# Kernel optimization log

Measured on AMD Instinct MI355X. Metric: run time of the kernel, lower is better.

The kernel has to match this reference:

```python
import jax, jax.numpy as jnp
import numpy as np

N, K, CI, CO = 1024, 16, 32, 32


def _elu(x):
    return jnp.where(x > 0, x, jnp.expm1(x))


def _eq22(adj, W, b):
    # adj: [B, D, m, m]; W: [15, D, S]; 15 permutation-equivariant basis ops (Maron et al.)
    B, D, m, _ = adj.shape
    mf = jnp.asarray(m, adj.dtype)
    eye = jnp.eye(m, dtype=adj.dtype)
    diag = jnp.diagonal(adj, axis1=2, axis2=3)          # [B,D,m]
    sr = adj.sum(3) / mf                                 # row sums
    sc = adj.sum(2) / mf                                 # col sums
    sd = diag.sum(-1) / mf                               # [B,D]
    sa = adj.sum((2, 3)) / (mf * mf)                     # [B,D]
    full = adj.shape
    bc = lambda t: jnp.broadcast_to(t, full)
    d2m = lambda v: v[..., :, None] * eye
    s2d = lambda s: s[..., None, None] * eye
    s2a = lambda s: jnp.broadcast_to(s[..., None, None], full)
    ops = jnp.stack([
        d2m(diag), s2d(sd), d2m(sr), d2m(sc), s2d(sa),
        bc(sc[..., None, :]), bc(sr[..., None, :]),
        bc(sc[..., :, None]), bc(sr[..., :, None]),
        adj, jnp.swapaxes(adj, 2, 3),
        bc(diag[..., None, :]), bc(diag[..., :, None]),
        s2a(sd), s2a(sa),
    ])  # [15,B,D,m,m]
    return jnp.einsum('pds,pbdij->bsij', W, ops) + b[None, :, None, None]


def _eq21(adj, W, b):
    # adj: [B,D,m,m] -> [B,S,m]; 5 basis ops
    m = adj.shape[-1]
    mf = jnp.asarray(m, adj.dtype)
    diag = jnp.diagonal(adj, axis1=2, axis2=3)
    sr = adj.sum(3) / mf
    sc = adj.sum(2) / mf
    sd = diag.sum(-1) / mf
    sa = adj.sum((2, 3)) / (mf * mf)
    vshape = diag.shape
    ops = jnp.stack([
        diag, sr, sc,
        jnp.broadcast_to(sd[..., None], vshape),
        jnp.broadcast_to(sa[..., None], vshape),
    ])
    return jnp.einsum('pds,pbdi->bsi', W, ops) + b[None, :, None]


def _eq12(x, W, b):
    # x: [B,D,m] -> [B,S,m,m]; 5 basis ops
    B, D, m = x.shape
    mf = jnp.asarray(m, x.dtype)
    eye = jnp.eye(m, dtype=x.dtype)
    s = x.sum(-1) / mf
    full = (B, D, m, m)
    ops = jnp.stack([
        x[..., :, None] * eye,
        s[..., None, None] * eye,
        jnp.broadcast_to(x[..., None, :], full),
        jnp.broadcast_to(x[..., :, None], full),
        jnp.broadcast_to(s[..., None, None], full),
    ])
    return jnp.einsum('pds,pbdij->bsij', W, ops) + b[None, :, None, None]


def _eq11(x, W, b):
    # x: [B,D,m] -> [B,S,m]; 2 basis ops
    mf = jnp.asarray(x.shape[-1], x.dtype)
    s = x.sum(-1) / mf
    ops = jnp.stack([x, jnp.broadcast_to(s[..., None], x.shape)])
    return jnp.einsum('pds,pbdi->bsi', W, ops) + b[None, :, None]


def _forward(x1, A, w22, b22, w21, b21, w12, b12, w11, b11, nbrs):
    n = x1.shape[0]
    # subgraph extraction: gather per-node neighbor features and dense sub-adjacency
    x_sub = jnp.transpose(x1[nbrs], (0, 2, 1))                                      # [N,Ci,K]
    adj_sub = jnp.transpose(A[nbrs[:, :, None], nbrs[:, None, :]], (0, 3, 1, 2))    # [N,Ci,K,K]
    adj_o = jnp.concatenate([_eq22(adj_sub, w22, b22), _eq12(x_sub, w12, b12)], axis=1)  # [N,2S,K,K]
    x_o = jnp.concatenate([_eq21(adj_sub, w21, b21), _eq11(x_sub, w11, b11)], axis=1)    # [N,2S,K]
    c2 = adj_o.shape[1]
    # scatter-mean subgraph edges back to global edge id = src*n + dst
    eid = (nbrs[:, :, None] * n + nbrs[:, None, :]).reshape(-1)
    ev = jnp.transpose(adj_o, (0, 2, 3, 1)).reshape(-1, c2)
    esum = jax.ops.segment_sum(ev, eid, num_segments=n * n)
    ecnt = jax.ops.segment_sum(jnp.ones(eid.shape, ev.dtype), eid, num_segments=n * n)
    edge_attr = _elu(esum / jnp.maximum(ecnt, 1.0)[:, None])
    # scatter-mean subgraph nodes back to global nodes
    nid = nbrs.reshape(-1)
    nv = jnp.transpose(x_o, (0, 2, 1)).reshape(-1, c2)
    nsum = jax.ops.segment_sum(nv, nid, num_segments=n)
    ncnt = jax.ops.segment_sum(jnp.ones(nid.shape, nv.dtype), nid, num_segments=n)
    x_nodes = _elu(nsum / jnp.maximum(ncnt, 1.0)[:, None])
    return edge_attr, x_nodes


def setup_inputs() -> dict:
    key = jax.random.key(0)
    ks = jax.random.split(key, 12)
    return {
        'x1': jax.random.normal(ks[0], (N, CI), jnp.float32),
        'A': jax.random.normal(ks[1], (N, N, CI), jnp.float32),
        'w22': jax.random.normal(ks[2], (15, CI, CO), jnp.float32) * 0.1,
        'b22': jax.random.normal(ks[3], (CO,), jnp.float32) * 0.1,
        'w21': jax.random.normal(ks[4], (5, CI, CO), jnp.float32) * 0.1,
        'b21': jax.random.normal(ks[5], (CO,), jnp.float32) * 0.1,
        'w12': jax.random.normal(ks[6], (5, CI, CO), jnp.float32) * 0.1,
        'b12': jax.random.normal(ks[7], (CO,), jnp.float32) * 0.1,
        'w11': jax.random.normal(ks[8], (2, CI, CO), jnp.float32) * 0.1,
        'b11': jax.random.normal(ks[9], (CO,), jnp.float32) * 0.1,
        'nbrs': jax.random.randint(ks[10], (N, K), 0, N),
    }


def reference(x1, A, w22, b22, w21, b21, w12, b12, w11, b11, nbrs):
    return _forward(x1, A, w22, b22, w21, b21, w12, b12, w11, b11, nbrs)
```

## Files before the change

kernel.cpp:

```cpp
#include <hip/hip_runtime.h>
#include <hip/hip_bf16.h>

#define NN 1024
#define KK 16
#define CI_ 32
#define CO_ 32
#define CAP 64
#define ECAP 8
#define DCAP 128
#define WLCAP 262144

__device__ __forceinline__ float elu_f(float x) {
    return x > 0.0f ? x : expm1f(x);
}

#define ECNT_OFF   0
#define DCNT_OFF   (1024*1024)
#define INVCNT_OFF (DCNT_OFF + 1024)
#define WLCNT_OFF  (INVCNT_OFF + 1024)
#define INVBUF_OFF (WLCNT_OFF + 1024)
#define WL_OFF     (INVBUF_OFF + 1024*CAP)
#define EBUF_OFF   (WL_OFF + WLCAP)
#define DBUF_OFF   (EBUF_OFF + 1024*1024*ECAP)
#define XSTG_OFF   (DBUF_OFF + 1024*DCAP)
#define ASTG_OFF   (XSTG_OFF + 1024*1024)

__global__ __launch_bounds__(256, 2) void subgraph_kernel(
    const float* __restrict__ x1, const float* __restrict__ A,
    const float* __restrict__ w22, const float* __restrict__ b22,
    const float* __restrict__ w21, const float* __restrict__ b21,
    const float* __restrict__ w12, const float* __restrict__ b12,
    const float* __restrict__ w11, const float* __restrict__ b11,
    const int* __restrict__ nbrs,
    float* __restrict__ adj_stage, float* __restrict__ x_stage,
    unsigned int* __restrict__ ecnt, unsigned int* __restrict__ dcnt,
    unsigned int* __restrict__ invcnt, unsigned int* __restrict__ invbuf,
    unsigned int* __restrict__ ebuf, unsigned int* __restrict__ dbuf,
    unsigned int* __restrict__ wlcnt, unsigned int* __restrict__ wl)
{
    const int b = blockIdx.x;
    const int t = threadIdx.x;

    __shared__ float adjS[32][257];
    __shared__ float xS[32][17];
    __shared__ float w10L[32][32];
    __shared__ float w11L[32][32];
    __shared__ float diagL[32][17], srL[32][17], scL[32][17];
    __shared__ float sdL[32], saL[32], sxL[32];
    __shared__ float rowp[32][17], colp[32][17], diagp[32][17];
    __shared__ float constp[32], dconst22[32];
    __shared__ float xi12[32][17], xj12[32][17], d12t[32][17];
    __shared__ float c12[32], dconst12[32];
    __shared__ float o21[32][17], o11[32][17];
    __shared__ int u[16];

    if (t < 16) u[t] = nbrs[b * KK + t];
    __syncthreads();

    if (t < 16) {
        unsigned int pos = atomicAdd(invcnt + u[t], 1u);
        if (pos < CAP) invbuf[(unsigned)u[t] * CAP + pos] = ((unsigned)b << 4) | (unsigned)t;
    }
    {
        const int pi = t >> 4, pj = t & 15;
        const unsigned vv = (unsigned)u[pi], ww = (unsigned)u[pj];
        const unsigned src = (unsigned)b * 256u + (unsigned)t;
        if (vv == ww) {
            unsigned pos = atomicAdd(dcnt + vv, 1u);
            if (pos < DCAP) dbuf[vv * DCAP + pos] = src;
        } else {
            const unsigned eid = vv * NN + ww;
            unsigned pos = atomicAdd(ecnt + eid, 1u);
            if (pos < ECAP) ebuf[(size_t)eid * ECAP + pos] = src;
            if (pos == 0u) {
                unsigned slot = atomicAdd(wlcnt, 1u);
                if (slot < WLCAP) wl[slot] = eid;
            }
        }
    }

    {
        const int pi = t >> 4, pj = t & 15;
        const float4* arow = reinterpret_cast<const float4*>(
            A + ((size_t)u[pi] * NN + (size_t)u[pj]) * CI_);
        #pragma unroll
        for (int q = 0; q < 8; ++q) {
            float4 r = arow[q];
            adjS[4*q+0][t] = r.x; adjS[4*q+1][t] = r.y;
            adjS[4*q+2][t] = r.z; adjS[4*q+3][t] = r.w;
        }
    }
    if (t < 128) {
        const int xi = t >> 3, q = t & 7;
        float4 v = reinterpret_cast<const float4*>(x1 + (size_t)u[xi] * CI_)[q];
        xS[4*q+0][xi] = v.x; xS[4*q+1][xi] = v.y;
        xS[4*q+2][xi] = v.z; xS[4*q+3][xi] = v.w;
    }
    for (int k = t; k < 1024; k += 256) {
        const int d = k >> 5, s = k & 31;
        w10L[d][s] = w22[9  * 1024 + k];
        w11L[d][s] = w22[10 * 1024 + k];
    }
    __syncthreads();

    {
        const int d = t & 31;
        for (int ii = t >> 5; ii < 16; ii += 8) {
            float s_r = 0.f, s_c = 0.f;
            #pragma unroll
            for (int jj = 0; jj < 16; ++jj) {
                s_r += adjS[d][ii * 16 + jj];
                s_c += adjS[d][jj * 16 + ii];
            }
            srL[d][ii] = s_r * (1.f / 16.f);
            scL[d][ii] = s_c * (1.f / 16.f);
            diagL[d][ii] = adjS[d][ii * 16 + ii];
        }
    }
    __syncthreads();
    if (t < 32) {
        float a = 0.f, dd = 0.f, xx = 0.f;
        #pragma unroll
        for (int ii = 0; ii < 16; ++ii) {
            a += srL[t][ii]; dd += diagL[t][ii]; xx += xS[t][ii];
        }
        saL[t] = a * (1.f / 16.f);
        sdL[t] = dd * (1.f / 16.f);
        sxL[t] = xx * (1.f / 16.f);
    }
    __syncthreads();

    {
        const int s = t & 31;
        for (int ii = t >> 5; ii < 16; ii += 8) {
            {
                float rp = 0.f, cp = 0.f, dp = 0.f, o21v = 0.f;
                #pragma unroll 4
                for (int d = 0; d < 32; ++d) {
                    const int wi = d * 32 + s;
                    const float di = diagL[d][ii], sr_ = srL[d][ii], sc_ = scL[d][ii];
                    rp   += w22[7*1024 + wi]*sc_ + w22[8*1024 + wi]*sr_ + w22[12*1024 + wi]*di;
                    cp   += w22[5*1024 + wi]*sc_ + w22[6*1024 + wi]*sr_ + w22[11*1024 + wi]*di;
                    dp   += w22[0*1024 + wi]*di  + w22[2*1024 + wi]*sr_ + w22[3*1024  + wi]*sc_;
                    o21v += w21[0*1024 + wi]*di  + w21[1*1024 + wi]*sr_ + w21[2*1024  + wi]*sc_
                          + w21[3*1024 + wi]*sdL[d] + w21[4*1024 + wi]*saL[d];
                }
                rowp[s][ii] = rp; colp[s][ii] = cp; diagp[s][ii] = dp;
                o21[s][ii]  = o21v + b21[s];
            }
            {
                float xiv = 0.f, xjv = 0.f, d12v = 0.f, o11v = 0.f;
                #pragma unroll 4
                for (int d = 0; d < 32; ++d) {
                    const int wi = d * 32 + s;
                    const float xv = xS[d][ii];
                    xjv  += w12[2*1024 + wi]*xv;
                    xiv  += w12[3*1024 + wi]*xv;
                    d12v += w12[0*1024 + wi]*xv;
                    o11v += w11[0*1024 + wi]*xv + w11[1*1024 + wi]*sxL[d];
                }
                xj12[s][ii] = xjv; xi12[s][ii] = xiv; d12t[s][ii] = d12v;
                o11[s][ii]  = o11v + b11[s];
            }
        }
        if (t < 32) {
            float cpv = 0.f, dc22 = 0.f, c12v = 0.f, dc12 = 0.f;
            #pragma unroll 4
            for (int d = 0; d < 32; ++d) {
                const int wi = d * 32 + t;
                cpv  += w22[13*1024 + wi]*sdL[d] + w22[14*1024 + wi]*saL[d];
                dc22 += w22[1*1024  + wi]*sdL[d] + w22[4*1024  + wi]*saL[d];
                c12v += w12[4*1024  + wi]*sxL[d];
                dc12 += w12[1*1024  + wi]*sxL[d];
            }
            constp[t]   = cpv + b22[t];
            dconst22[t] = dc22;
            c12[t]      = c12v + b12[t];
            dconst12[t] = dc12;
        }
    }
    __syncthreads();

    {
        const int pi = t >> 4, pj = t & 15;
        const bool isdiag = (pi == pj);
        const int pt = pj * 16 + pi;
        float4* e4 = reinterpret_cast<float4*>(adj_stage + ((size_t)b * 256 + t) * 64);

        #pragma unroll
        for (int h = 0; h < 2; ++h) {
            float acc[16];
            #pragma unroll
            for (int s16 = 0; s16 < 16; ++s16) {
                const int s = h * 16 + s16;
                float v = rowp[s][pi] + colp[s][pj] + constp[s];
                if (isdiag) v += diagp[s][pi] + dconst22[s];
                acc[s16] = v;
            }
            #pragma unroll 8
            for (int d = 0; d < 32; ++d) {
                const float a  = adjS[d][t];
                const float at = adjS[d][pt];
                #pragma unroll
                for (int s16 = 0; s16 < 16; ++s16)
                    acc[s16] = fmaf(a, w10L[d][h*16+s16], fmaf(at, w11L[d][h*16+s16], acc[s16]));
            }
            #pragma unroll
            for (int q = 0; q < 4; ++q)
                e4[h*4 + q] = make_float4(acc[4*q], acc[4*q+1], acc[4*q+2], acc[4*q+3]);
        }

        #pragma unroll
        for (int q = 0; q < 8; ++q) {
            float vv[4];
            #pragma unroll
            for (int r = 0; r < 4; ++r) {
                const int s = 4*q + r;
                float v = xj12[s][pj] + xi12[s][pi] + c12[s];
                if (isdiag) v += d12t[s][pi] + dconst12[s];
                vv[r] = v;
            }
            e4[8 + q] = make_float4(vv[0], vv[1], vv[2], vv[3]);
        }
    }

    for (int k = t; k < 1024; k += 256) {
        const int ii = k >> 6, c = k & 63;
        const float v = (c < 32) ? o21[c][ii] : o11[c - 32][ii];
        x_stage[((size_t)b * 16 + ii) * 64 + c] = v;
    }
}

__global__ __launch_bounds__(256) void finalize_kernel(
    const float* __restrict__ adj_stage, const float* __restrict__ x_stage,
    const unsigned int* __restrict__ ecnt, const unsigned int* __restrict__ dcnt,
    const unsigned int* __restrict__ invcnt, const unsigned int* __restrict__ invbuf,
    const unsigned int* __restrict__ ebuf, const unsigned int* __restrict__ dbuf,
    const unsigned int* __restrict__ wlcnt, const unsigned int* __restrict__ wl,
    float* __restrict__ out)
{
    const int bid = blockIdx.x;
    if (bid < 65536) {
        const unsigned gid = (unsigned)bid * 256u + (unsigned)threadIdx.x;
        const unsigned eid = gid >> 4, ln = gid & 15u;
        const unsigned v = eid >> 10, w = eid & 1023u;
        const unsigned cnt = (v == w) ? dcnt[v] : ecnt[eid];
        if (cnt == 0u)
            reinterpret_cast<float4*>(out + (size_t)eid * 64)[ln] =
                make_float4(0.f, 0.f, 0.f, 0.f);
        return;
    }

    const int grp = threadIdx.x >> 4;
    const int ln  = threadIdx.x & 15;
    const unsigned gidx = (unsigned)(bid - 65536) * 16u + (unsigned)grp;

    if (gidx < WLCAP) {
        unsigned nwl = *wlcnt; if (nwl > WLCAP) nwl = WLCAP;
        if (gidx >= nwl) return;
        const unsigned eid = wl[gidx];
        const unsigned full = ecnt[eid];
        unsigned cnt = full; if (cnt > ECAP) cnt = ECAP;
        const unsigned* list = ebuf + (size_t)eid * ECAP;
        float4 acc = make_float4(0.f, 0.f, 0.f, 0.f);
        for (unsigned p = 0; p < cnt; ++p) {
            const unsigned src = list[p];
            float4 f = reinterpret_cast<const float4*>(adj_stage + (size_t)src * 64)[ln];
            acc.x += f.x; acc.y += f.y; acc.z += f.z; acc.w += f.w;
        }
        const float inv = 1.0f / (float)full;
        acc.x = elu_f(acc.x * inv); acc.y = elu_f(acc.y * inv);
        acc.z = elu_f(acc.z * inv); acc.w = elu_f(acc.w * inv);
        reinterpret_cast<float4*>(out + (size_t)eid * 64)[ln] = acc;
    } else if (gidx < WLCAP + 1024u) {
        const unsigned v = gidx - WLCAP;
        const unsigned full = dcnt[v];
        if (full == 0u) return;
        unsigned cnt = full; if (cnt > DCAP) cnt = DCAP;
        const unsigned* list = dbuf + v * DCAP;
        float4 acc = make_float4(0.f, 0.f, 0.f, 0.f);
        for (unsigned p = 0; p < cnt; ++p) {
            const unsigned src = list[p];
            float4 f = reinterpret_cast<const float4*>(adj_stage + (size_t)src * 64)[ln];
            acc.x += f.x; acc.y += f.y; acc.z += f.z; acc.w += f.w;
        }
        const float inv = 1.0f / (float)full;
        acc.x = elu_f(acc.x * inv); acc.y = elu_f(acc.y * inv);
        acc.z = elu_f(acc.z * inv); acc.w = elu_f(acc.w * inv);
        const unsigned eid = (v << 10) | v;
        reinterpret_cast<float4*>(out + (size_t)eid * 64)[ln] = acc;
    } else if (gidx < WLCAP + 2048u) {
        const unsigned v = gidx - WLCAP - 1024u;
        const unsigned full = invcnt[v];
        unsigned cnt = full; if (cnt > CAP) cnt = CAP;
        float4 acc = make_float4(0.f, 0.f, 0.f, 0.f);
        for (unsigned p = 0; p < cnt; ++p) {
            const unsigned e = invbuf[v * CAP + p];
            float4 f = reinterpret_cast<const float4*>(x_stage + (size_t)e * 64)[ln];
            acc.x += f.x; acc.y += f.y; acc.z += f.z; acc.w += f.w;
        }
        const float inv = full ? 1.0f / (float)full : 0.0f;
        acc.x = elu_f(acc.x * inv); acc.y = elu_f(acc.y * inv);
        acc.z = elu_f(acc.z * inv); acc.w = elu_f(acc.w * inv);
        reinterpret_cast<float4*>(out + (size_t)NN * NN * 64 + (size_t)v * 64)[ln] = acc;
    }
}

extern "C" void kernel_launch(void* const* d_in, const int* in_sizes, int n_in,
                              void* d_out, int out_size, void* d_ws, size_t ws_size,
                              hipStream_t stream) {
    (void)in_sizes; (void)n_in; (void)out_size; (void)ws_size;
    const float* x1   = (const float*)d_in[0];
    const float* A    = (const float*)d_in[1];
    const float* w22  = (const float*)d_in[2];
    const float* b22  = (const float*)d_in[3];
    const float* w21  = (const float*)d_in[4];
    const float* b21  = (const float*)d_in[5];
    const float* w12  = (const float*)d_in[6];
    const float* b12  = (const float*)d_in[7];
    const float* w11  = (const float*)d_in[8];
    const float* b11  = (const float*)d_in[9];
    const int*   nbrs = (const int*)d_in[10];

    float* out = (float*)d_out;
    unsigned int* ws_u = (unsigned int*)d_ws;
    unsigned int* ecnt   = ws_u + ECNT_OFF;
    unsigned int* dcnt   = ws_u + DCNT_OFF;
    unsigned int* invcnt = ws_u + INVCNT_OFF;
    unsigned int* wlcnt  = ws_u + WLCNT_OFF;
    unsigned int* invbuf = ws_u + INVBUF_OFF;
    unsigned int* wl     = ws_u + WL_OFF;
    unsigned int* ebuf   = ws_u + EBUF_OFF;
    unsigned int* dbuf   = ws_u + DBUF_OFF;
    float* x_stage   = (float*)(ws_u + XSTG_OFF);
    float* adj_stage = (float*)(ws_u + ASTG_OFF);

    hipMemsetAsync(ecnt, 0, (size_t)(1024 * 1024 + 3072) * sizeof(unsigned int), stream);

    subgraph_kernel<<<NN, 256, 0, stream>>>(
        x1, A, w22, b22, w21, b21, w12, b12, w11, b11, nbrs,
        adj_stage, x_stage, ecnt, dcnt, invcnt, invbuf, ebuf, dbuf, wlcnt, wl);

    const int gblocks = 65536 + (WLCAP + 2048) / 16;
    finalize_kernel<<<gblocks, 256, 0, stream>>>(
        adj_stage, x_stage, ecnt, dcnt, invcnt, invbuf, ebuf, dbuf, wlcnt, wl, out);
}
```

Measured before the change: 557.4 us.

## Pad adjacency tile, batch weight loads, drop weight LDS copies, split finalize kernel

Several changes land together in the subgraph kernel. The adjacency tile is padded to a stride of 17 per row to avoid LDS bank conflicts on transposed reads, and the nbrs indices are read straight into registers, removing one barrier. The projection loop now loads weights once per d and covers two rows, and x_stage is written directly. The w10/w11 LDS copies are dropped in favour of global (cached) reads in the hot FMA loop. The finalize kernel is split into separate zero-fill and gather launches, which adds a launch but removes the branch on block index.

```diff
diff --git a/kernel.cpp b/kernel.cpp
--- a/kernel.cpp
+++ b/kernel.cpp
@@ -40,30 +40,26 @@
 {
     const int b = blockIdx.x;
     const int t = threadIdx.x;
-
-    __shared__ float adjS[32][257];
+    const int pi = t >> 4, pj = t & 15;
+
+    __shared__ float adjS[32][273];
     __shared__ float xS[32][17];
-    __shared__ float w10L[32][32];
-    __shared__ float w11L[32][32];
     __shared__ float diagL[32][17], srL[32][17], scL[32][17];
     __shared__ float sdL[32], saL[32], sxL[32];
     __shared__ float rowp[32][17], colp[32][17], diagp[32][17];
     __shared__ float constp[32], dconst22[32];
     __shared__ float xi12[32][17], xj12[32][17], d12t[32][17];
     __shared__ float c12[32], dconst12[32];
-    __shared__ float o21[32][17], o11[32][17];
-    __shared__ int u[16];
-
-    if (t < 16) u[t] = nbrs[b * KK + t];
-    __syncthreads();
+
+    const int upi = nbrs[b * KK + pi];
+    const int upj = nbrs[b * KK + pj];
 
     if (t < 16) {
-        unsigned int pos = atomicAdd(invcnt + u[t], 1u);
-        if (pos < CAP) invbuf[(unsigned)u[t] * CAP + pos] = ((unsigned)b << 4) | (unsigned)t;
-    }
-    {
-        const int pi = t >> 4, pj = t & 15;
-        const unsigned vv = (unsigned)u[pi], ww = (unsigned)u[pj];
+        unsigned pos = atomicAdd(invcnt + upj, 1u);
+        if (pos < CAP) invbuf[(unsigned)upj * CAP + pos] = ((unsigned)b << 4) | (unsigned)t;
+    }
+    {
+        const unsigned vv = (unsigned)upi, ww = (unsigned)upj;
         const unsigned src = (unsigned)b * 256u + (unsigned)t;
         if (vv == ww) {
             unsigned pos = atomicAdd(dcnt + vv, 1u);
@@ -80,26 +76,22 @@
     }
 
     {
-        const int pi = t >> 4, pj = t & 15;
         const float4* arow = reinterpret_cast<const float4*>(
-            A + ((size_t)u[pi] * NN + (size_t)u[pj]) * CI_);
+            A + ((size_t)upi * NN + (size_t)upj) * CI_);
+        const int base = pi * 17 + pj;
         #pragma unroll
         for (int q = 0; q < 8; ++q) {
             float4 r = arow[q];
-            adjS[4*q+0][t] = r.x; adjS[4*q+1][t] = r.y;
-            adjS[4*q+2][t] = r.z; adjS[4*q+3][t] = r.w;
+            adjS[4*q+0][base] = r.x; adjS[4*q+1][base] = r.y;
+            adjS[4*q+2][base] = r.z; adjS[4*q+3][base] = r.w;
         }
     }
     if (t < 128) {
         const int xi = t >> 3, q = t & 7;
-        float4 v = reinterpret_cast<const float4*>(x1 + (size_t)u[xi] * CI_)[q];
+        const int ux = nbrs[b * KK + xi];
+        float4 v = reinterpret_cast<const float4*>(x1 + (size_t)ux * CI_)[q];
         xS[4*q+0][xi] = v.x; xS[4*q+1][xi] = v.y;
         xS[4*q+2][xi] = v.z; xS[4*q+3][xi] = v.w;
-    }
-    for (int k = t; k < 1024; k += 256) {
-        const int d = k >> 5, s = k & 31;
-        w10L[d][s] = w22[9  * 1024 + k];
-        w11L[d][s] = w22[10 * 1024 + k];
     }
     __syncthreads();
 
@@ -109,12 +101,12 @@
             float s_r = 0.f, s_c = 0.f;
             #pragma unroll
             for (int jj = 0; jj < 16; ++jj) {
-                s_r += adjS[d][ii * 16 + jj];
-                s_c += adjS[d][jj * 16 + ii];
+                s_r += adjS[d][ii * 17 + jj];
+                s_c += adjS[d][jj * 17 + ii];
             }
             srL[d][ii] = s_r * (1.f / 16.f);
             scL[d][ii] = s_c * (1.f / 16.f);
-            diagL[d][ii] = adjS[d][ii * 16 + ii];
+            diagL[d][ii] = adjS[d][ii * 18];
         }
     }
     __syncthreads();
@@ -131,37 +123,46 @@
     __syncthreads();
 
     {
-        const int s = t & 31;
-        for (int ii = t >> 5; ii < 16; ii += 8) {
-            {
-                float rp = 0.f, cp = 0.f, dp = 0.f, o21v = 0.f;
-                #pragma unroll 4
-                for (int d = 0; d < 32; ++d) {
-                    const int wi = d * 32 + s;
-                    const float di = diagL[d][ii], sr_ = srL[d][ii], sc_ = scL[d][ii];
-                    rp   += w22[7*1024 + wi]*sc_ + w22[8*1024 + wi]*sr_ + w22[12*1024 + wi]*di;
-                    cp   += w22[5*1024 + wi]*sc_ + w22[6*1024 + wi]*sr_ + w22[11*1024 + wi]*di;
-                    dp   += w22[0*1024 + wi]*di  + w22[2*1024 + wi]*sr_ + w22[3*1024  + wi]*sc_;
-                    o21v += w21[0*1024 + wi]*di  + w21[1*1024 + wi]*sr_ + w21[2*1024  + wi]*sc_
-                          + w21[3*1024 + wi]*sdL[d] + w21[4*1024 + wi]*saL[d];
-                }
-                rowp[s][ii] = rp; colp[s][ii] = cp; diagp[s][ii] = dp;
-                o21[s][ii]  = o21v + b21[s];
-            }
-            {
-                float xiv = 0.f, xjv = 0.f, d12v = 0.f, o11v = 0.f;
-                #pragma unroll 4
-                for (int d = 0; d < 32; ++d) {
-                    const int wi = d * 32 + s;
-                    const float xv = xS[d][ii];
-                    xjv  += w12[2*1024 + wi]*xv;
-                    xiv  += w12[3*1024 + wi]*xv;
-                    d12v += w12[0*1024 + wi]*xv;
-                    o11v += w11[0*1024 + wi]*xv + w11[1*1024 + wi]*sxL[d];
-                }
-                xj12[s][ii] = xjv; xi12[s][ii] = xiv; d12t[s][ii] = d12v;
-                o11[s][ii]  = o11v + b11[s];
-            }
+        const int s  = t & 31;
+        const int i0 = t >> 5;
+        float rp[2] = {0.f, 0.f}, cp[2] = {0.f, 0.f}, dp[2] = {0.f, 0.f};
+        float ov[2] = {0.f, 0.f}, o1v[2] = {0.f, 0.f};
+        float xj[2] = {0.f, 0.f}, xiv[2] = {0.f, 0.f}, dv[2] = {0.f, 0.f};
+        #pragma unroll 2
+        for (int d = 0; d < 32; ++d) {
+            const int wi = d * 32 + s;
+            const float a0  = w22[0*1024 + wi], a2  = w22[2*1024 + wi];
+            const float a3  = w22[3*1024 + wi], a5  = w22[5*1024 + wi];
+            const float a6  = w22[6*1024 + wi], a7  = w22[7*1024 + wi];
+            const float a8  = w22[8*1024 + wi], a11 = w22[11*1024 + wi];
+            const float a12 = w22[12*1024 + wi];
+            const float g0 = w21[0*1024 + wi], g1 = w21[1*1024 + wi];
+            const float g2 = w21[2*1024 + wi], g3 = w21[3*1024 + wi];
+            const float g4 = w21[4*1024 + wi];
+            const float q0 = w12[0*1024 + wi], q2 = w12[2*1024 + wi];
+            const float q3 = w12[3*1024 + wi];
+            const float h0 = w11[0*1024 + wi], h1 = w11[1*1024 + wi];
+            const float sdd = sdL[d], saa = saL[d], sxx = sxL[d];
+            #pragma unroll
+            for (int k = 0; k < 2; ++k) {
+                const int ii = i0 + 8 * k;
+                const float di = diagL[d][ii], sr_ = srL[d][ii], sc_ = scL[d][ii];
+                const float xv = xS[d][ii];
+                rp[k]  += a7*sc_ + a8*sr_ + a12*di;
+                cp[k]  += a5*sc_ + a6*sr_ + a11*di;
+                dp[k]  += a0*di  + a2*sr_ + a3*sc_;
+                ov[k]  += g0*di + g1*sr_ + g2*sc_ + g3*sdd + g4*saa;
+                xj[k]  += q2*xv; xiv[k] += q3*xv; dv[k] += q0*xv;
+                o1v[k] += h0*xv + h1*sxx;
+            }
+        }
+        #pragma unroll
+        for (int k = 0; k < 2; ++k) {
+            const int ii = i0 + 8 * k;
+            rowp[s][ii] = rp[k]; colp[s][ii] = cp[k]; diagp[s][ii] = dp[k];
+            xj12[s][ii] = xj[k]; xi12[s][ii] = xiv[k]; d12t[s][ii] = dv[k];
+            x_stage[((size_t)b * 16 + ii) * 64 + s]      = ov[k]  + b21[s];
+            x_stage[((size_t)b * 16 + ii) * 64 + 32 + s] = o1v[k] + b11[s];
         }
         if (t < 32) {
             float cpv = 0.f, dc22 = 0.f, c12v = 0.f, dc12 = 0.f;
@@ -182,9 +183,9 @@
     __syncthreads();
 
     {
-        const int pi = t >> 4, pj = t & 15;
         const bool isdiag = (pi == pj);
-        const int pt = pj * 16 + pi;
+        const int idx  = pi * 17 + pj;
+        const int idxT = pj * 17 + pi;
         float4* e4 = reinterpret_cast<float4*>(adj_stage + ((size_t)b * 256 + t) * 64);
 
         #pragma unroll
@@ -197,13 +198,15 @@
                 if (isdiag) v += diagp[s][pi] + dconst22[s];
                 acc[s16] = v;
             }
-            #pragma unroll 8
+            #pragma unroll 4
             for (int d = 0; d < 32; ++d) {
-                const float a  = adjS[d][t];
-                const float at = adjS[d][pt];
+                const float a  = adjS[d][idx];
+                const float at = adjS[d][idxT];
+                const float* w9r  = w22 + 9*1024  + d*32 + h*16;
+                const float* w10r = w22 + 10*1024 + d*32 + h*16;
                 #pragma unroll
                 for (int s16 = 0; s16 < 16; ++s16)
-                    acc[s16] = fmaf(a, w10L[d][h*16+s16], fmaf(at, w11L[d][h*16+s16], acc[s16]));
+                    acc[s16] = fmaf(a, w9r[s16], fmaf(at, w10r[s16], acc[s16]));
             }
             #pragma unroll
             for (int q = 0; q < 4; ++q)
@@ -223,15 +226,22 @@
             e4[8 + q] = make_float4(vv[0], vv[1], vv[2], vv[3]);
         }
     }
-
-    for (int k = t; k < 1024; k += 256) {
-        const int ii = k >> 6, c = k & 63;
-        const float v = (c < 32) ? o21[c][ii] : o11[c - 32][ii];
-        x_stage[((size_t)b * 16 + ii) * 64 + c] = v;
-    }
-}
-
-__global__ __launch_bounds__(256) void finalize_kernel(
+}
+
+__global__ __launch_bounds__(256) void zero_fill_kernel(
+    const unsigned int* __restrict__ ecnt, const unsigned int* __restrict__ dcnt,
+    float* __restrict__ out)
+{
+    const unsigned gid = (unsigned)blockIdx.x * 256u + (unsigned)threadIdx.x;
+    const unsigned eid = gid >> 4, ln = gid & 15u;
+    const unsigned v = eid >> 10, w = eid & 1023u;
+    const unsigned cnt = (v == w) ? dcnt[v] : ecnt[eid];
+    if (cnt == 0u)
+        reinterpret_cast<float4*>(out + (size_t)eid * 64)[ln] =
+            make_float4(0.f, 0.f, 0.f, 0.f);
+}
+
+__global__ __launch_bounds__(256) void gather_kernel(
     const float* __restrict__ adj_stage, const float* __restrict__ x_stage,
     const unsigned int* __restrict__ ecnt, const unsigned int* __restrict__ dcnt,
     const unsigned int* __restrict__ invcnt, const unsigned int* __restrict__ invbuf,
@@ -239,21 +249,9 @@
     const unsigned int* __restrict__ wlcnt, const unsigned int* __restrict__ wl,
     float* __restrict__ out)
 {
-    const int bid = blockIdx.x;
-    if (bid < 65536) {
-        const unsigned gid = (unsigned)bid * 256u + (unsigned)threadIdx.x;
-        const unsigned eid = gid >> 4, ln = gid & 15u;
-        const unsigned v = eid >> 10, w = eid & 1023u;
-        const unsigned cnt = (v == w) ? dcnt[v] : ecnt[eid];
-        if (cnt == 0u)
-            reinterpret_cast<float4*>(out + (size_t)eid * 64)[ln] =
-                make_float4(0.f, 0.f, 0.f, 0.f);
-        return;
-    }
-
     const int grp = threadIdx.x >> 4;
     const int ln  = threadIdx.x & 15;
-    const unsigned gidx = (unsigned)(bid - 65536) * 16u + (unsigned)grp;
+    const unsigned gidx = (unsigned)blockIdx.x * 16u + (unsigned)grp;
 
     if (gidx < WLCAP) {
         unsigned nwl = *wlcnt; if (nwl > WLCAP) nwl = WLCAP;
@@ -341,7 +339,8 @@
         x1, A, w22, b22, w21, b21, w12, b12, w11, b11, nbrs,
         adj_stage, x_stage, ecnt, dcnt, invcnt, invbuf, ebuf, dbuf, wlcnt, wl);
 
-    const int gblocks = 65536 + (WLCAP + 2048) / 16;
-    finalize_kernel<<<gblocks, 256, 0, stream>>>(
+    zero_fill_kernel<<<65536, 256, 0, stream>>>(ecnt, dcnt, out);
+
+    gather_kernel<<<(WLCAP + 2048) / 16, 256, 0, stream>>>(
         adj_stage, x_stage, ecnt, dcnt, invcnt, invbuf, ebuf, dbuf, wlcnt, wl, out);
 }
```

Result: no change. 553.1 us (-0.8%).
